# Performance work log

Hardware: AMD Instinct MI355X
Metric: run time of the kernel (lower is better)

Reference implementation:

```python
import jax, jax.numpy as jnp
import numpy as np

NUM_RANGES = 31   # bins [0,1)...[29,30) plus [30, inf) -> max_height=30
EPS = 1e-06
ALPHA = 0.5
NAN_VALUE = -1.0


def setup_inputs() -> dict:
    key = jax.random.key(0)
    k1, k2 = jax.random.split(key)
    shape = (64, 512, 512)
    # targets in log1p space; natural heights expm1(target) span [0, ~34)
    target = jax.random.uniform(k1, shape, dtype=jnp.float32) * 3.55
    pred = target + 0.1 * jax.random.normal(k2, shape, dtype=jnp.float32)
    return {"pred": pred, "target": target}


def reference(pred, target):
    valid = target != NAN_VALUE                      # no-data mask
    natural = jnp.expm1(target)                      # heights in natural space
    # arithmetic bin index: ranges [i, i+1) for i<30, last bin [30, inf)
    bin_idx = jnp.clip(jnp.floor(natural), 0.0, NUM_RANGES - 1).astype(jnp.int32)
    in_range = natural >= 0.0                        # samples below 0 fall in no range

    # histogram of valid, in-range samples (scatter-add)
    counts = jnp.zeros(NUM_RANGES, jnp.float32).at[bin_idx.ravel()].add(
        (valid & in_range).ravel().astype(jnp.float32))
    total_valid = jnp.sum(valid).astype(jnp.float32)
    denom = jnp.maximum(total_valid, 1.0)
    freq = counts / denom
    w = 1.0 / (freq ** ALPHA + EPS)                  # inverse-frequency weights, [31]

    base = jnp.abs(pred - target)                    # L1 in log1p space
    sample_w = jnp.where(in_range, w[bin_idx], 0.0)  # gather per-sample weight
    weighted = base * sample_w
    # mean over valid samples (out-of-range valid samples contribute 0, as in torch)
    mean_loss = jnp.sum(jnp.where(valid, weighted, 0.0)) / denom
    return mean_loss
```

## Files before the change

### kernel.cpp

```cpp
#include <hip/hip_runtime.h>
#include <math.h>

#define NBINS 31
#define NCOPIES 256
#define BLOCK 256
#define GRID 1024

#define CNT_SHIFT 25
#define SUM_MASK  0x1FFFFFFu
#define FIX_SCALE 32768.0f


__device__ __forceinline__ void bin_accum(float p, float t,
                                          unsigned* my_hist, unsigned& my_valid)
{
    bool valid = (t != -1.0f);
    my_valid += valid ? 1u : 0u;
    float nat = __expf(t) - 1.0f;
    if (valid && nat >= 0.0f) {
        int b = (int)fminf(nat, 30.0f);
        unsigned pk = (1u << CNT_SHIFT)
                    | (unsigned)(fabsf(p - t) * FIX_SCALE + 0.5f);
        my_hist[b] += pk;
    }
}

__global__ __launch_bounds__(BLOCK) void zero_ws_kernel(unsigned* ws)
{
    int t = threadIdx.x;
    if (t < 192) ws[t] = 0u;
}

__global__ __launch_bounds__(BLOCK) void hist_kernel(
    const float* __restrict__ pred, const float* __restrict__ target, int n,
    float* __restrict__ g_sums, unsigned* __restrict__ g_cnts,
    unsigned* __restrict__ g_total)
{
    __shared__ unsigned s_hist[NCOPIES * NBINS];
    __shared__ float    p_sum[NBINS * 8];
    __shared__ unsigned p_cnt[NBINS * 8];
    __shared__ unsigned s_tot[BLOCK / 64];

    const int tid = threadIdx.x;
    for (int i = tid; i < NCOPIES * NBINS; i += BLOCK) s_hist[i] = 0u;
    __syncthreads();

    unsigned* my_hist = s_hist + tid * NBINS;
    unsigned  my_valid = 0;

    const int n4 = n >> 2;
    const float4* __restrict__ pred4 = (const float4*)pred;
    const float4* __restrict__ targ4 = (const float4*)target;
    const int gstride = gridDim.x * BLOCK;

    for (int i = blockIdx.x * BLOCK + tid; i < n4; i += gstride) {
        float4 p = pred4[i];
        float4 t = targ4[i];
        bin_accum(p.x, t.x, my_hist, my_valid);
        bin_accum(p.y, t.y, my_hist, my_valid);
        bin_accum(p.z, t.z, my_hist, my_valid);
        bin_accum(p.w, t.w, my_hist, my_valid);
    }
    for (int i = (n4 << 2) + blockIdx.x * BLOCK + tid; i < n; i += gstride) {
        bin_accum(pred[i], target[i], my_hist, my_valid);
    }
    __syncthreads();

    if (tid < NBINS * 8) {
        int b = tid >> 3, g = tid & 7;
        float fs = 0.0f; unsigned cs = 0u;
        for (int k = 0; k < 32; ++k) {
            unsigned v = s_hist[(g * 32 + k) * NBINS + b];
            cs += v >> CNT_SHIFT;
            fs += (float)(v & SUM_MASK);
        }
        p_sum[b * 8 + g] = fs;
        p_cnt[b * 8 + g] = cs;
    }
    unsigned v = my_valid;
    #pragma unroll
    for (int off = 32; off >= 1; off >>= 1) v += __shfl_down(v, off, 64);
    if ((tid & 63) == 0) s_tot[tid >> 6] = v;
    __syncthreads();

    if (tid < NBINS) {
        float fs = 0.0f; unsigned cs = 0u;
        #pragma unroll
        for (int g = 0; g < 8; ++g) { fs += p_sum[tid * 8 + g]; cs += p_cnt[tid * 8 + g]; }
        atomicAdd(&g_sums[tid], fs * (1.0f / FIX_SCALE));
        atomicAdd(&g_cnts[tid], cs);
    }
    if (tid == 0) {
        unsigned tot = 0;
        #pragma unroll
        for (int w = 0; w < BLOCK / 64; ++w) tot += s_tot[w];
        atomicAdd(g_total, tot);
    }
}

__global__ void finalize_kernel(const float* __restrict__ g_sums,
                                const unsigned* __restrict__ g_cnts,
                                const unsigned* __restrict__ g_total,
                                float* __restrict__ out)
{
    int lane = threadIdx.x;
    float denom = fmaxf((float)(*g_total), 1.0f);
    float contrib = 0.0f;
    if (lane < NBINS) {
        float freq = (float)g_cnts[lane] / denom;
        float w = 1.0f / (sqrtf(freq) + 1e-6f);
        contrib = g_sums[lane] * w;
    }
    #pragma unroll
    for (int off = 32; off >= 1; off >>= 1) contrib += __shfl_down(contrib, off, 64);
    if (lane == 0) *out = contrib / denom;
}

extern "C" void kernel_launch(void* const* d_in, const int* in_sizes, int n_in,
                              void* d_out, int out_size, void* d_ws, size_t ws_size,
                              hipStream_t stream)
{
    const float* pred   = (const float*)d_in[0];
    const float* target = (const float*)d_in[1];
    float* out = (float*)d_out;
    int n = in_sizes[0];

    float*    g_sums  = (float*)d_ws;
    unsigned* g_cnts  = (unsigned*)d_ws + 64;
    unsigned* g_total = (unsigned*)d_ws + 128;

    zero_ws_kernel<<<1, BLOCK, 0, stream>>>((unsigned*)d_ws);

    hist_kernel<<<GRID, BLOCK, 0, stream>>>(pred, target, n, g_sums, g_cnts, g_total);

    finalize_kernel<<<1, 64, 0, stream>>>(g_sums, g_cnts, g_total, out);
}
```

Measured before the change: 158.0 us.

## Transpose LDS histogram to bin-major layout with batched asm read-modify-write

```diff
diff --git a/kernel.cpp b/kernel.cpp
--- a/kernel.cpp
+++ b/kernel.cpp
@@ -2,6 +2,7 @@
 #include <math.h>
 
 #define NBINS 31
+#define NSLOT 32
 #define NCOPIES 256
 #define BLOCK 256
 #define GRID 1024
@@ -11,18 +12,56 @@
 #define FIX_SCALE 32768.0f
 
 
-__device__ __forceinline__ void bin_accum(float p, float t,
-                                          unsigned* my_hist, unsigned& my_valid)
+__device__ __forceinline__ void prep(float p, float t, unsigned hbase,
+                                     unsigned& addr, unsigned& pk, unsigned& nvalid)
 {
-    bool valid = (t != -1.0f);
-    my_valid += valid ? 1u : 0u;
+    nvalid += (t != -1.0f) ? 1u : 0u;
+    bool ok = (t >= 0.0f);
     float nat = __expf(t) - 1.0f;
-    if (valid && nat >= 0.0f) {
-        int b = (int)fminf(nat, 30.0f);
-        unsigned pk = (1u << CNT_SHIFT)
-                    | (unsigned)(fabsf(p - t) * FIX_SCALE + 0.5f);
-        my_hist[b] += pk;
-    }
+    unsigned b = (unsigned)(int)fminf(nat, 30.0f);
+    unsigned pkv = (1u << CNT_SHIFT)
+                 | (unsigned)(fabsf(p - t) * FIX_SCALE + 0.5f);
+    pk   = ok ? pkv : 0u;
+    addr = hbase + ((ok ? b : 31u) << 10);
+}
+
+__device__ __forceinline__ void packet(float4 p, float4 t, unsigned hbase,
+                                       unsigned& nvalid)
+{
+    unsigned a0, a1, a2, a3, k0, k1, k2, k3;
+    prep(p.x, t.x, hbase, a0, k0, nvalid);
+    prep(p.y, t.y, hbase, a1, k1, nvalid);
+    prep(p.z, t.z, hbase, a2, k2, nvalid);
+    prep(p.w, t.w, hbase, a3, k3, nvalid);
+
+    unsigned r0, r1, r2, r3;
+    asm volatile(
+        "ds_read_b32 %0, %4\n\t"
+        "ds_read_b32 %1, %5\n\t"
+        "ds_read_b32 %2, %6\n\t"
+        "ds_read_b32 %3, %7"
+        : "=&v"(r0), "=&v"(r1), "=&v"(r2), "=&v"(r3)
+        : "v"(a0), "v"(a1), "v"(a2), "v"(a3));
+
+    unsigned s0 = k0;
+    unsigned s1 = k1 + (a1 == a0 ? s0 : 0u);
+    unsigned s2 = k2 + (a2 == a1 ? s1 : (a2 == a0 ? s0 : 0u));
+    unsigned s3 = k3 + (a3 == a2 ? s2 : (a3 == a1 ? s1 : (a3 == a0 ? s0 : 0u)));
+
+    asm volatile(
+        "s_waitcnt lgkmcnt(0)\n\t"
+        "v_add_u32 %0, %0, %4\n\t"
+        "v_add_u32 %1, %1, %5\n\t"
+        "v_add_u32 %2, %2, %6\n\t"
+        "v_add_u32 %3, %3, %7\n\t"
+        "ds_write_b32 %8, %0\n\t"
+        "ds_write_b32 %9, %1\n\t"
+        "ds_write_b32 %10, %2\n\t"
+        "ds_write_b32 %11, %3"
+        : "+v"(r0), "+v"(r1), "+v"(r2), "+v"(r3)
+        : "v"(s0), "v"(s1), "v"(s2), "v"(s3),
+          "v"(a0), "v"(a1), "v"(a2), "v"(a3)
+        : "memory");
 }
 
 __global__ __launch_bounds__(BLOCK) void zero_ws_kernel(unsigned* ws)
@@ -36,48 +75,71 @@
     float* __restrict__ g_sums, unsigned* __restrict__ g_cnts,
     unsigned* __restrict__ g_total)
 {
-    __shared__ unsigned s_hist[NCOPIES * NBINS];
+    __shared__ unsigned s_hist[NSLOT * NCOPIES];
     __shared__ float    p_sum[NBINS * 8];
     __shared__ unsigned p_cnt[NBINS * 8];
     __shared__ unsigned s_tot[BLOCK / 64];
 
     const int tid = threadIdx.x;
-    for (int i = tid; i < NCOPIES * NBINS; i += BLOCK) s_hist[i] = 0u;
+    for (int i = tid; i < NSLOT * NCOPIES; i += BLOCK) s_hist[i] = 0u;
     __syncthreads();
 
-    unsigned* my_hist = s_hist + tid * NBINS;
-    unsigned  my_valid = 0;
+    const unsigned hbase = (unsigned)(uintptr_t)(void*)s_hist + ((unsigned)tid << 2);
+    unsigned nvalid = 0;
 
     const int n4 = n >> 2;
     const float4* __restrict__ pred4 = (const float4*)pred;
     const float4* __restrict__ targ4 = (const float4*)target;
-    const int gstride = gridDim.x * BLOCK;
+    const int st = gridDim.x * BLOCK;
+    const int i0 = blockIdx.x * BLOCK + tid;
 
-    for (int i = blockIdx.x * BLOCK + tid; i < n4; i += gstride) {
-        float4 p = pred4[i];
-        float4 t = targ4[i];
-        bin_accum(p.x, t.x, my_hist, my_valid);
-        bin_accum(p.y, t.y, my_hist, my_valid);
-        bin_accum(p.z, t.z, my_hist, my_valid);
-        bin_accum(p.w, t.w, my_hist, my_valid);
+    if (n4 > 0) {
+        float4 pA, tA, pB, tB;
+        {
+            int ia = (i0      < n4) ? i0      : 0;
+            int ib = (i0 + st < n4) ? i0 + st : 0;
+            pA = pred4[ia]; tA = targ4[ia];
+            pB = pred4[ib]; tB = targ4[ib];
+        }
+        for (int i = i0; i < n4; i += 2 * st) {
+            int ca = (i + 2 * st < n4) ? i + 2 * st : 0;
+            int cb = (i + 3 * st < n4) ? i + 3 * st : 0;
+            float4 pNA = pred4[ca], tNA = targ4[ca];
+            packet(pA, tA, hbase, nvalid);
+            float4 pNB = pred4[cb], tNB = targ4[cb];
+            if (i + st < n4) packet(pB, tB, hbase, nvalid);
+            pA = pNA; tA = tNA; pB = pNB; tB = tNB;
+        }
     }
-    for (int i = (n4 << 2) + blockIdx.x * BLOCK + tid; i < n; i += gstride) {
-        bin_accum(pred[i], target[i], my_hist, my_valid);
+    for (int i = (n4 << 2) + i0; i < n; i += st) {
+        float p = pred[i], t = target[i];
+        nvalid += (t != -1.0f) ? 1u : 0u;
+        if (t >= 0.0f) {
+            float nat = __expf(t) - 1.0f;
+            int b = (int)fminf(nat, 30.0f);
+            s_hist[b * NCOPIES + tid] += (1u << CNT_SHIFT)
+                | (unsigned)(fabsf(p - t) * FIX_SCALE + 0.5f);
+        }
     }
+    asm volatile("s_waitcnt lgkmcnt(0)" ::: "memory");
     __syncthreads();
 
     if (tid < NBINS * 8) {
-        int b = tid >> 3, g = tid & 7;
+        const int b = tid >> 3, g = tid & 7;
+        const uint4* row = (const uint4*)(s_hist + b * NCOPIES);
         float fs = 0.0f; unsigned cs = 0u;
-        for (int k = 0; k < 32; ++k) {
-            unsigned v = s_hist[(g * 32 + k) * NBINS + b];
-            cs += v >> CNT_SHIFT;
-            fs += (float)(v & SUM_MASK);
+        #pragma unroll
+        for (int kk = 0; kk < 8; ++kk) {
+            uint4 v = row[g + 8 * kk];
+            cs += (v.x >> CNT_SHIFT) + (v.y >> CNT_SHIFT)
+                + (v.z >> CNT_SHIFT) + (v.w >> CNT_SHIFT);
+            fs += (float)(v.x & SUM_MASK) + (float)(v.y & SUM_MASK)
+                + (float)(v.z & SUM_MASK) + (float)(v.w & SUM_MASK);
         }
-        p_sum[b * 8 + g] = fs;
-        p_cnt[b * 8 + g] = cs;
+        p_sum[tid] = fs;
+        p_cnt[tid] = cs;
     }
-    unsigned v = my_valid;
+    unsigned v = nvalid;
     #pragma unroll
     for (int off = 32; off >= 1; off >>= 1) v += __shfl_down(v, off, 64);
     if ((tid & 63) == 0) s_tot[tid >> 6] = v;
```

Measured after the change: 149.6 us. 5.3% less time.
